# Performance work log

Measured on AMD Instinct MI355X. Metric: run time of the kernel, lower is better.

## Reference

```python
import jax, jax.numpy as jnp
import numpy as np

T, MEM, B, DM, N, D = 1024, 1024, 4, 1024, 16, 64
C = MEM + T
SCALE = 1.0 / D ** 0.5
LN_EPS = 1e-5


def _rel_shift(x):
    # x: [T, C, B, N] -> Transformer-XL relative shift
    t, c = x.shape[0], x.shape[1]
    zero_pad = jnp.zeros((t, 1) + x.shape[2:], x.dtype)
    x_padded = jnp.concatenate([zero_pad, x], axis=1)  # [T, C+1, B, N]
    x_padded = x_padded.reshape((c + 1, t) + x.shape[2:])
    return x_padded[1:].reshape(x.shape)


def setup_inputs() -> dict:
    key = jax.random.key(0)
    ks = jax.random.split(key, 8)
    h = jax.random.normal(ks[0], (T, B, DM), jnp.float32)
    m = jax.random.normal(ks[1], (MEM, B, DM), jnp.float32)
    r = jax.random.normal(ks[2], (C, DM), jnp.float32)
    # causal mask with memory: query i (global pos MEM+i) may attend to j <= MEM+i
    mask = (jnp.arange(C)[None, :] > (jnp.arange(T)[:, None] + MEM))[:, :, None]  # [T,C,1] bool, True=disallow
    W_qkv = jax.random.normal(ks[3], (DM, 3 * N * D), jnp.float32) * 0.02
    W_r = jax.random.normal(ks[4], (DM, N * D), jnp.float32) * 0.02
    W_o = jax.random.normal(ks[5], (N * D, DM), jnp.float32) * 0.02
    r_w_bias = jax.random.normal(ks[6], (N, D), jnp.float32)
    r_r_bias = jax.random.normal(ks[7], (N, D), jnp.float32)
    ln_gamma = jnp.ones((DM,), jnp.float32)
    ln_beta = jnp.zeros((DM,), jnp.float32)
    return {"h": h, "m": m, "r": r, "mask": mask, "W_qkv": W_qkv, "W_r": W_r,
            "W_o": W_o, "r_w_bias": r_w_bias, "r_r_bias": r_r_bias,
            "ln_gamma": ln_gamma, "ln_beta": ln_beta}


def reference(h, m, r, mask, W_qkv, W_r, W_o, r_w_bias, r_r_bias, ln_gamma, ln_beta):
    t, b = h.shape[0], h.shape[1]
    c = r.shape[0]
    cat = jnp.concatenate([m, h], axis=0)          # [C, B, DM]
    w_heads = cat @ W_qkv                           # [C, B, 3*N*D]
    w_q, w_k, w_v = jnp.split(w_heads, 3, axis=-1)
    w_q = w_q[-t:].reshape(t, b, N, D)              # [T,B,N,D]
    w_k = w_k.reshape(c, b, N, D)                   # [C,B,N,D]
    w_v = w_v.reshape(c, b, N, D)                   # [C,B,N,D]
    r_k = (r @ W_r).reshape(c, N, D)                # [C,N,D]
    AC = jnp.einsum('ibnd,jbnd->ijbn', w_q + r_w_bias, w_k)
    BD = jnp.einsum('ibnd,jnd->ijbn', w_q + r_r_bias, r_k)
    BD = _rel_shift(BD)
    score = (AC + BD) * SCALE                       # [T,C,B,N]
    score = jnp.where(mask[:, :, :, None], jnp.float32(-65000.0), score.astype(jnp.float32)).astype(score.dtype)
    prob = jax.nn.softmax(score, axis=1)
    vec = jnp.einsum('ijbn,jbnd->ibnd', prob, w_v).reshape(t, b, N * D)
    attn_out = vec @ W_o                            # [T,B,DM]
    x = h + attn_out
    mu = jnp.mean(x, axis=-1, keepdims=True)
    var = jnp.mean((x - mu) ** 2, axis=-1, keepdims=True)
    return (x - mu) * jax.lax.rsqrt(var + LN_EPS) * ln_gamma + ln_beta
```

## Files before the change

### kernel.cpp

```cpp
#include <hip/hip_runtime.h>
#include <stdint.h>

#define T_LEN 1024
#define MEM_LEN 1024
#define C_LEN 2048
#define B_SZ 4
#define DM_ 1024
#define NH 16
#define HD 64

typedef __attribute__((ext_vector_type(8))) short short8;
typedef __attribute__((ext_vector_type(4))) float f32x4;
typedef __attribute__((ext_vector_type(4))) unsigned short ushort4v;
typedef __attribute__((ext_vector_type(8))) unsigned short ushort8v;
typedef __attribute__((ext_vector_type(4))) float float4v;

__device__ __forceinline__ unsigned short f2bf(float f) {
  union { float f; unsigned int u; } v; v.f = f;
  unsigned int r = v.u + 0x7fffu + ((v.u >> 16) & 1u);
  return (unsigned short)(r >> 16);
}
__device__ __forceinline__ float bf2f(unsigned short b) {
  union { unsigned int u; float f; } v; v.u = ((unsigned int)b) << 16;
  return v.f;
}
__device__ __forceinline__ unsigned int cvtpk(float lo, float hi) {
  unsigned int r;
  asm("v_cvt_pk_bf16_f32 %0, %1, %2" : "=v"(r) : "v"(lo), "v"(hi));
  return r;
}
__device__ __forceinline__ f32x4 mfma16(short8 a, short8 b, f32x4 c) {
  return __builtin_amdgcn_mfma_f32_16x16x32_bf16(a, b, c, 0, 0, 0);
}

__global__ void k_convert_all(const float* __restrict__ m, const float* __restrict__ h,
                              const float* __restrict__ r,
                              unsigned short* __restrict__ catB,
                              unsigned short* __restrict__ rB) {
  int idx = blockIdx.x * 256 + threadIdx.x;
  const int MQ = (MEM_LEN * B_SZ * DM_) / 4;
  const int CQ = 2 * MQ;
  float4v v;
  unsigned short* dst;
  int di;
  if (idx < MQ)      { v = ((const float4v*)m)[idx];       dst = catB; di = idx; }
  else if (idx < CQ) { v = ((const float4v*)h)[idx - MQ];  dst = catB; di = idx; }
  else               { v = ((const float4v*)r)[idx - CQ];  dst = rB;   di = idx - CQ; }
  ushort4v o;
  o.x = f2bf(v.x); o.y = f2bf(v.y); o.z = f2bf(v.z); o.w = f2bf(v.w);
  ((ushort4v*)dst)[di] = o;
}

__global__ void k_transpose_w(const float* __restrict__ Wqkv, const float* __restrict__ Wr,
                              const float* __restrict__ Wo,
                              unsigned short* __restrict__ WqkvT, unsigned short* __restrict__ WrT,
                              unsigned short* __restrict__ WoT) {
  __shared__ float tile[32][33];
  const int z = blockIdx.z;
  const int Ccols = (z == 0) ? 3072 : 1024;
  if (blockIdx.x * 32 >= Ccols) return;
  const float* in = (z == 0) ? Wqkv : (z == 1) ? Wr : Wo;
  unsigned short* out = (z == 0) ? WqkvT : (z == 1) ? WrT : WoT;
  int c0 = blockIdx.x * 32, r0 = blockIdx.y * 32;
  int tx = threadIdx.x & 31, ty = threadIdx.x >> 5;
#pragma unroll
  for (int p = 0; p < 4; ++p)
    tile[ty + 8 * p][tx] = in[(size_t)(r0 + ty + 8 * p) * Ccols + c0 + tx];
  __syncthreads();
#pragma unroll
  for (int p = 0; p < 4; ++p)
    out[(size_t)(c0 + ty + 8 * p) * 1024 + r0 + tx] = f2bf(tile[tx][ty + 8 * p]);
}

template <int MODE>
__global__ __launch_bounds__(256) void k_gemm(const unsigned short* __restrict__ A,
                                              const unsigned short* __restrict__ BT,
                                              void* __restrict__ out1, void* __restrict__ out2,
                                              int M, int N, int K, int ldc) {
  __shared__ unsigned short As[128 * 64];
  __shared__ unsigned short Bs[128 * 64];
  const int tid = threadIdx.x;
  const int w = tid >> 6, l = tid & 63;
  const int wm = w >> 1, wn = w & 1;
  const int lg = l >> 4, lr = l & 15;
  const int gx = gridDim.x;
  const int pid = blockIdx.y * gx + blockIdx.x;
  const int xcd = pid & 7;
  const int idx = pid >> 3;
  const int cb = idx % gx;
  const int rb = (idx / gx) * 8 + xcd;
  const int m0 = rb * 128, n0 = cb * 128;
  f32x4 acc[4][4] = {};
  const int lrow8 = l >> 3;
  const int scol = (l & 7) * 8;
  const unsigned short* Abase = A + (size_t)m0 * K;
  const unsigned short* Bbase = BT + (size_t)n0 * K;
  for (int kt = 0; kt < K; kt += 64) {
    __syncthreads();
#pragma unroll
    for (int q = 0; q < 4; ++q) {
      int chunk = w * 4 + q;
      int row = chunk * 8 + lrow8;
      __builtin_amdgcn_global_load_lds(
          (const __attribute__((address_space(1))) void*)(Abase + (size_t)row * K + kt + scol),
          (__attribute__((address_space(3))) void*)(As + chunk * 512), 16, 0, 0);
      __builtin_amdgcn_global_load_lds(
          (const __attribute__((address_space(1))) void*)(Bbase + (size_t)row * K + kt + scol),
          (__attribute__((address_space(3))) void*)(Bs + chunk * 512), 16, 0, 0);
    }
    __syncthreads();
#pragma unroll
    for (int ks = 0; ks < 2; ++ks) {
      short8 a[4], bb[4];
#pragma unroll
      for (int mi = 0; mi < 4; ++mi)
        a[mi] = *(const short8*)&As[(wm * 64 + mi * 16 + lr) * 64 + ks * 32 + lg * 8];
#pragma unroll
      for (int ni = 0; ni < 4; ++ni)
        bb[ni] = *(const short8*)&Bs[(wn * 64 + ni * 16 + lr) * 64 + ks * 32 + lg * 8];
#pragma unroll
      for (int mi = 0; mi < 4; ++mi)
#pragma unroll
        for (int ni = 0; ni < 4; ++ni)
          acc[mi][ni] = mfma16(a[mi], bb[ni], acc[mi][ni]);
    }
  }
#pragma unroll
  for (int mi = 0; mi < 4; ++mi)
#pragma unroll
    for (int ni = 0; ni < 4; ++ni)
#pragma unroll
      for (int r = 0; r < 4; ++r) {
        int row = m0 + wm * 64 + mi * 16 + lg * 4 + r;
        int cc = n0 + wn * 64 + ni * 16 + lr;
        float val = acc[mi][ni][r];
        if (MODE == 1) {
          ((float*)out1)[(size_t)row * ldc + cc] = val;
        } else if (MODE == 2) {
          int nn = (cc & 1023) >> 6, d = cc & 63;
          int c = row >> 2, b = row & 3;
          size_t addr = ((size_t)((b * 16 + nn) * 2048 + c)) * 64 + d;
          unsigned short* dst = (cc < 1024) ? (unsigned short*)out1 : (unsigned short*)out2;
          dst[addr] = f2bf(val);
        } else if (MODE == 3) {
          int nn = cc >> 6, d = cc & 63;
          int t = row >> 2, b = row & 3;
          ((unsigned short*)out1)[((size_t)((b * 16 + nn) * 1024 + t)) * 64 + d] = f2bf(val);
        } else {
          int nn = cc >> 6, d = cc & 63;
          ((unsigned short*)out1)[((size_t)(nn * 2048 + row)) * 64 + d] = f2bf(val);
        }
      }
}

__global__ void k_vt(const unsigned short* __restrict__ Vp, unsigned short* __restrict__ VT) {
  __shared__ unsigned short tile[64][72];
  int c0 = blockIdx.x * 64;
  int n = blockIdx.y, b = blockIdx.z;
  int t = threadIdx.x;
  const unsigned short* src = Vp + ((size_t)((b * 16 + n) * 2048 + c0)) * 64;
#pragma unroll
  for (int p = 0; p < 16; ++p) {
    int idx = p * 256 + t;
    int r = idx >> 6, d = idx & 63;
    tile[d][r] = src[(size_t)r * 64 + d];
  }
  __syncthreads();
#pragma unroll
  for (int p = 0; p < 16; ++p) {
    int idx = p * 256 + t;
    int d = idx >> 6, c = idx & 63;
    VT[(size_t)((b * 16 + n) * 64 + d) * 2048 + c0 + c] = tile[d][c];
  }
}

__device__ __forceinline__ void stage_tile(const unsigned short* __restrict__ Kbase,
                                           const unsigned short* __restrict__ Vbase,
                                           unsigned short* ksBuf, unsigned short* vsBuf,
                                           int j0, int tid) {
#pragma unroll
  for (int q = 0; q < 2; ++q) {
    int chunk = q * 256 + tid;
    int row = chunk >> 3;
    int slot = chunk & 7;
    int ss = slot ^ (row & 7);
    __builtin_amdgcn_global_load_lds(
        (const __attribute__((address_space(1))) void*)(Kbase + (size_t)(j0 + row) * 64 + ss * 8),
        (__attribute__((address_space(3))) void*)(ksBuf + chunk * 8), 16, 0, 0);
    __builtin_amdgcn_global_load_lds(
        (const __attribute__((address_space(1))) void*)(Vbase + (size_t)row * 2048 + j0 + ss * 8),
        (__attribute__((address_space(3))) void*)(vsBuf + chunk * 8), 16, 0, 0);
  }
}

__global__ __launch_bounds__(256) void k_attn(const unsigned short* __restrict__ Qp,
                                              const unsigned short* __restrict__ Kp,
                                              const unsigned short* __restrict__ VT,
                                              const unsigned short* __restrict__ Rkp,
                                              const float* __restrict__ rwb,
                                              const float* __restrict__ rrb,
                                              unsigned short* __restrict__ po,
                                              float* __restrict__ psumG) {
  __shared__ __align__(16) unsigned short Ks[2][64 * 64];
  __shared__ __align__(16) unsigned short Vs[2][64 * 64];
  __shared__ unsigned short P[4][16][72];
  const int tid = threadIdx.x;
  const int w = tid >> 6, l = tid & 63;
  const int lg = l >> 4, lr = l & 15;
  const int L = blockIdx.x;
  const int bnlo = L & 7;
  const int rest = L >> 3;
  const int bnhi = rest / 48;
  const int inner = rest - bnhi * 48;
  const int xt = inner / 3;
  const int s  = inner - xt * 3;
  const int bn = bnhi * 8 + bnlo;
  const int i0 = xt * 64;
  const int n = bn & 15, b = bn >> 4;
  const int wrow = i0 + w * 16;

  const int ntile = xt + 17;
  const int t0 = (s * ntile) / 3;
  const int t1 = ((s + 1) * ntile) / 3;

  const unsigned short* Kbase = Kp + (size_t)bn * 2048 * 64;
  const unsigned short* Vbase = VT + (size_t)bn * 64 * 2048;
  const unsigned short* Rkbase = Rkp + (size_t)n * 2048 * 64;

  short8 aq0u, aq1u, aq0v, aq1v;
  {
    const unsigned short* qp = Qp + (size_t)(bn * 1024 + wrow + lr) * 64 + lg * 8;
    short8 q0 = *(const short8*)qp;
    short8 q1 = *(const short8*)(qp + 32);
    const float* up = rwb + n * 64 + lg * 8;
    const float* vp = rrb + n * 64 + lg * 8;
#pragma unroll
    for (int e = 0; e < 8; ++e) {
      float q0f = bf2f((unsigned short)q0[e]);
      float q1f = bf2f((unsigned short)q1[e]);
      aq0u[e] = (short)f2bf(q0f + up[e]);
      aq1u[e] = (short)f2bf(q1f + up[e + 32]);
      aq0v[e] = (short)f2bf(q0f + vp[e]);
      aq1v[e] = (short)f2bf(q1f + vp[e + 32]);
    }
  }
  float psum[4];
  f32x4 o[4];
#pragma unroll
  for (int r = 0; r < 4; ++r) psum[r] = 0.f;
#pragma unroll
  for (int df = 0; df < 4; ++df) o[df] = (f32x4){0.f, 0.f, 0.f, 0.f};

  stage_tile(Kbase, Vbase, Ks[0], Vs[0], t0 * 64, tid);
  stage_tile(Kbase, Vbase, Ks[1], Vs[1], (t0 + 1) * 64, tid);

  const float EXPC = 0.18033688011112042f;

  for (int jt = t0; jt < t1; ++jt) {
    const int j0 = jt * 64;
    const int cur = (jt - t0) & 1;
    if (jt + 1 < t1) { asm volatile("s_waitcnt vmcnt(4)" ::: "memory"); }
    else             { asm volatile("s_waitcnt vmcnt(0)" ::: "memory"); }
    __builtin_amdgcn_s_barrier();

    f32x4 sac[4];
#pragma unroll
    for (int jf = 0; jf < 4; ++jf) sac[jf] = (f32x4){0.f, 0.f, 0.f, 0.f};
    __builtin_amdgcn_s_setprio(1);
#pragma unroll
    for (int jf = 0; jf < 4; ++jf) {
      int row = jf * 16 + lr;
      int rx = row & 7;
      short8 k0 = *(const short8*)&Ks[cur][row * 64 + ((lg ^ rx) * 8)];
      short8 k1 = *(const short8*)&Ks[cur][row * 64 + (((4 + lg) ^ rx) * 8)];
      sac[jf] = mfma16(aq0u, k0, sac[jf]);
      sac[jf] = mfma16(aq1u, k1, sac[jf]);
    }
    __builtin_amdgcn_s_setprio(0);
    const int kbw = j0 + 1008 - i0 - w * 16;
    f32x4 gb[5];
#pragma unroll
    for (int jg = 0; jg < 5; ++jg) {
      int rowK = kbw + jg * 16 + lr;
      short8 b0 = {}, b1 = {};
      if (rowK < C_LEN) {
        const unsigned short* rp = Rkbase + (size_t)rowK * 64 + lg * 8;
        b0 = *(const short8*)rp;
        b1 = *(const short8*)(rp + 32);
      }
      f32x4 g = (f32x4){0.f, 0.f, 0.f, 0.f};
      g = mfma16(aq0v, b0, g);
      g = mfma16(aq1v, b1, g);
      gb[jg] = g;
    }
    const bool needMask = (j0 + 63 > i0 + w * 16 + MEM_LEN);
    float p[4][4];
#pragma unroll
    for (int r = 0; r < 4; ++r) {
      const int R = lg * 4 + r;
      const int delta = lr + 15 - R;
      const int src = (l & 48) | (delta & 15);
      float v0 = __shfl(gb[0][r], src);
      float v1 = __shfl(gb[1][r], src);
      float v2 = __shfl(gb[2][r], src);
      float v3 = __shfl(gb[3][r], src);
      float v4 = __shfl(gb[4][r], src);
      const bool hi = delta >= 16;
      float bd0 = hi ? v1 : v0;
      float bd1 = hi ? v2 : v1;
      float bd2 = hi ? v3 : v2;
      float bd3 = hi ? v4 : v3;
      float e0 = exp2f((sac[0][r] + bd0) * EXPC);
      float e1 = exp2f((sac[1][r] + bd1) * EXPC);
      float e2 = exp2f((sac[2][r] + bd2) * EXPC);
      float e3 = exp2f((sac[3][r] + bd3) * EXPC);
      if (needMask) {
        const int jlim = i0 + w * 16 + R + MEM_LEN;
        int j = j0 + lr;
        e0 = (j > jlim) ? 0.f : e0;  j += 16;
        e1 = (j > jlim) ? 0.f : e1;  j += 16;
        e2 = (j > jlim) ? 0.f : e2;  j += 16;
        e3 = (j > jlim) ? 0.f : e3;
      }
      p[0][r] = e0; p[1][r] = e1; p[2][r] = e2; p[3][r] = e3;
    }
#pragma unroll
    for (int jf = 0; jf < 4; ++jf)
#pragma unroll
      for (int r = 0; r < 4; ++r) psum[r] += p[jf][r];
#pragma unroll
    for (int r = 0; r < 4; ++r) {
      unsigned int a01 = cvtpk(p[0][r], p[1][r]);
      unsigned int a23 = cvtpk(p[2][r], p[3][r]);
      const int R = lg * 4 + r;
      P[w][R][lr]      = (unsigned short)a01;
      P[w][R][16 + lr] = (unsigned short)(a01 >> 16);
      P[w][R][32 + lr] = (unsigned short)a23;
      P[w][R][48 + lr] = (unsigned short)(a23 >> 16);
    }
    __builtin_amdgcn_s_setprio(1);
#pragma unroll
    for (int ks = 0; ks < 2; ++ks) {
      short8 ap = *(const short8*)&P[w][lr][ks * 32 + lg * 8];
#pragma unroll
      for (int df = 0; df < 4; ++df) {
        int row = df * 16 + lr;
        int rx = row & 7;
        short8 vv = *(const short8*)&Vs[cur][row * 64 + (((ks * 4 + lg) ^ rx) * 8)];
        o[df] = mfma16(ap, vv, o[df]);
      }
    }
    __builtin_amdgcn_s_setprio(0);
    __builtin_amdgcn_s_barrier();
    if (jt + 2 < t1)
      stage_tile(Kbase, Vbase, Ks[cur], Vs[cur], (jt + 2) * 64, tid);
  }
  const int pbase = (bn * 16 + xt) * 3 + s;
  unsigned short* poB = po + (size_t)pbase * 4096;
#pragma unroll
  for (int r = 0; r < 4; ++r) {
    float v = psum[r];
    v += __shfl_xor(v, 1);
    v += __shfl_xor(v, 2);
    v += __shfl_xor(v, 4);
    v += __shfl_xor(v, 8);
    if (lr == 0) psumG[pbase * 64 + w * 16 + lg * 4 + r] = v;
  }
#pragma unroll
  for (int df = 0; df < 4; ++df)
#pragma unroll
    for (int r = 0; r < 4; ++r)
      poB[(w * 16 + lg * 4 + r) * 64 + df * 16 + lr] = f2bf(o[df][r]);
}

__global__ __launch_bounds__(256) void k_ared(const unsigned short* __restrict__ po,
                                              const float* __restrict__ psumG,
                                              unsigned short* __restrict__ vec) {
  const int idx = blockIdx.x;
  const int tid = threadIdx.x;
  const int bn = idx >> 4, xt = idx & 15;
  const int b = bn >> 4, n = bn & 15;
  __shared__ float rs[64];
  if (tid < 64) {
    const float* q = psumG + idx * 192;
    rs[tid] = q[tid] + q[tid + 64] + q[tid + 128];
  }
  __syncthreads();
  const ushort8v* p0 = (const ushort8v*)(po + (size_t)(idx * 3 + 0) * 4096);
  const ushort8v* p1 = (const ushort8v*)(po + (size_t)(idx * 3 + 1) * 4096);
  const ushort8v* p2 = (const ushort8v*)(po + (size_t)(idx * 3 + 2) * 4096);
#pragma unroll
  for (int k = 0; k < 2; ++k) {
    int e = tid + k * 256;
    int row = e >> 3, d8 = e & 7;
    ushort8v a = p0[e], bb = p1[e], c = p2[e];
    float inv = 1.f / rs[row];
    int t = xt * 64 + row;
    ushort8v ov;
#pragma unroll
    for (int q = 0; q < 8; ++q)
      ov[q] = f2bf((bf2f(a[q]) + bf2f(bb[q]) + bf2f(c[q])) * inv);
    *(ushort8v*)&vec[(size_t)(t * 4 + b) * 1024 + n * 64 + d8 * 8] = ov;
  }
}

__global__ __launch_bounds__(256) void k_ln(const float* __restrict__ xg, const float* __restrict__ h,
                                            const float* __restrict__ gamma, const float* __restrict__ beta,
                                            float* __restrict__ out) {
  const int row = blockIdx.x;
  const int t = threadIdx.x;
  __shared__ float red1[4], red2[4];
  float4v xv = ((const float4v*)(xg + (size_t)row * 1024))[t];
  float4v hv = ((const float4v*)(h + (size_t)row * 1024))[t];
  float x0 = xv.x + hv.x, x1 = xv.y + hv.y, x2 = xv.z + hv.z, x3 = xv.w + hv.w;
  float s = x0 + x1 + x2 + x3;
#pragma unroll
  for (int off = 1; off < 64; off <<= 1) s += __shfl_xor(s, off);
  if ((t & 63) == 0) red1[t >> 6] = s;
  __syncthreads();
  float mean = (red1[0] + red1[1] + red1[2] + red1[3]) * (1.f / 1024.f);
  float d0 = x0 - mean, d1 = x1 - mean, d2 = x2 - mean, d3 = x3 - mean;
  float q = d0 * d0 + d1 * d1 + d2 * d2 + d3 * d3;
#pragma unroll
  for (int off = 1; off < 64; off <<= 1) q += __shfl_xor(q, off);
  if ((t & 63) == 0) red2[t >> 6] = q;
  __syncthreads();
  float var = (red2[0] + red2[1] + red2[2] + red2[3]) * (1.f / 1024.f);
  float rs = rsqrtf(var + 1e-5f);
  float4v gv = ((const float4v*)gamma)[t];
  float4v bv = ((const float4v*)beta)[t];
  float4v ov;
  ov.x = d0 * rs * gv.x + bv.x;
  ov.y = d1 * rs * gv.y + bv.y;
  ov.z = d2 * rs * gv.z + bv.z;
  ov.w = d3 * rs * gv.w + bv.w;
  ((float4v*)(out + (size_t)row * 1024))[t] = ov;
}

extern "C" void kernel_launch(void* const* d_in, const int* in_sizes, int n_in,
                              void* d_out, int out_size, void* d_ws, size_t ws_size,
                              hipStream_t stream) {
  (void)in_sizes; (void)n_in; (void)out_size; (void)ws_size;
  const float* h    = (const float*)d_in[0];
  const float* m    = (const float*)d_in[1];
  const float* r    = (const float*)d_in[2];
  const float* Wqkv = (const float*)d_in[4];
  const float* Wr   = (const float*)d_in[5];
  const float* Wo   = (const float*)d_in[6];
  const float* rwb  = (const float*)d_in[7];
  const float* rrb  = (const float*)d_in[8];
  const float* gam  = (const float*)d_in[9];
  const float* bet  = (const float*)d_in[10];
  float* out = (float*)d_out;

  char* ws = (char*)d_ws;
  unsigned short* catB   = (unsigned short*)(ws + 0);
  unsigned short* WqkvT  = (unsigned short*)(ws + 16777216);
  unsigned short* WrT    = (unsigned short*)(ws + 23068672);
  unsigned short* WoT    = (unsigned short*)(ws + 25165824);
  unsigned short* Vp     = (unsigned short*)(ws + 27262976);
  unsigned short* po     = (unsigned short*)(ws + 44040192);
  unsigned short* VT     = (unsigned short*)(ws + 81788928);
  unsigned short* vec    = (unsigned short*)(ws + 99221504);
  float* xbuf            = (float*)(ws + 107610112);
  unsigned short* rB     = (unsigned short*)(ws + 124387328);
  unsigned short* Kp     = (unsigned short*)(ws + 128581632);
  unsigned short* Qp     = (unsigned short*)(ws + 145358848);
  unsigned short* Rkp    = (unsigned short*)(ws + 153747456);
  float* psumG = (float*)(ws + 124387328);

  hipLaunchKernelGGL(k_convert_all, dim3(10240), dim3(256), 0, stream, m, h, r, catB, rB);
  hipLaunchKernelGGL(k_transpose_w, dim3(96, 32, 3), dim3(256), 0, stream,
                     Wqkv, Wr, Wo, WqkvT, WrT, WoT);
  hipLaunchKernelGGL(k_gemm<2>, dim3(16, 64), dim3(256), 0, stream,
                     catB, WqkvT + (size_t)1024 * 1024, (void*)Kp, (void*)Vp, 8192, 2048, 1024, 0);
  hipLaunchKernelGGL(k_gemm<3>, dim3(8, 32), dim3(256), 0, stream,
                     catB + (size_t)4096 * 1024, WqkvT, (void*)Qp, nullptr, 4096, 1024, 1024, 0);
  hipLaunchKernelGGL(k_gemm<4>, dim3(8, 16), dim3(256), 0, stream,
                     rB, WrT, (void*)Rkp, nullptr, 2048, 1024, 1024, 0);
  hipLaunchKernelGGL(k_vt, dim3(32, 16, 4), dim3(256), 0, stream, Vp, VT);
  hipLaunchKernelGGL(k_attn, dim3(3072), dim3(256), 0, stream, Qp, Kp, VT, Rkp, rwb, rrb, po, psumG);
  hipLaunchKernelGGL(k_ared, dim3(1024), dim3(256), 0, stream, po, psumG, vec);
  hipLaunchKernelGGL(k_gemm<1>, dim3(8, 32), dim3(256), 0, stream,
                     vec, WoT, (void*)xbuf, nullptr, 4096, 1024, 1024, 1024);
  hipLaunchKernelGGL(k_ln, dim3(4096), dim3(256), 0, stream, xbuf, h, gam, bet, out);
}
```

Baseline: 322.9 us.

## Merge QKV/R projection GEMMs into one launch and single-buffer V in attention

The three projection GEMMs (K/V, Q, R) are merged into one grouped launch of 1408 blocks, with the block index choosing the mode. This removes two launch tails and lets the small GEMMs fill the GPU alongside the large one. In the attention kernel, V becomes single-buffered and is staged one tile ahead, separately from K, which stays double-buffered. An extra waitcnt and barrier before the PV MFMA step cut LDS use, possibly raising occupancy, at the cost of exposing V load latency and an extra barrier per tile. The s_setprio hints are also removed.

```diff
diff --git a/kernel.cpp b/kernel.cpp
--- a/kernel.cpp
+++ b/kernel.cpp
@@ -72,11 +72,96 @@
     out[(size_t)(c0 + ty + 8 * p) * 1024 + r0 + tx] = f2bf(tile[tx][ty + 8 * p]);
 }
 
-template <int MODE>
-__global__ __launch_bounds__(256) void k_gemm(const unsigned short* __restrict__ A,
-                                              const unsigned short* __restrict__ BT,
-                                              void* __restrict__ out1, void* __restrict__ out2,
-                                              int M, int N, int K, int ldc) {
+__global__ __launch_bounds__(256) void k_gemm_qkv(const unsigned short* __restrict__ catB,
+                                                  const unsigned short* __restrict__ rB,
+                                                  const unsigned short* __restrict__ WqkvT,
+                                                  const unsigned short* __restrict__ WrT,
+                                                  unsigned short* __restrict__ Kp,
+                                                  unsigned short* __restrict__ Vp,
+                                                  unsigned short* __restrict__ Qp,
+                                                  unsigned short* __restrict__ Rkp) {
+  __shared__ unsigned short As[128 * 64];
+  __shared__ unsigned short Bs[128 * 64];
+  const int tid = threadIdx.x;
+  const int w = tid >> 6, l = tid & 63;
+  const int wm = w >> 1, wn = w & 1;
+  const int lg = l >> 4, lr = l & 15;
+  const int bid = blockIdx.x;
+  int mode, lpid, gx;
+  const unsigned short *A, *BT;
+  if (bid < 1024)      { mode = 2; lpid = bid;        gx = 16; A = catB;                        BT = WqkvT + (size_t)1024 * 1024; }
+  else if (bid < 1280) { mode = 3; lpid = bid - 1024; gx = 8;  A = catB + (size_t)4096 * 1024;  BT = WqkvT; }
+  else                 { mode = 4; lpid = bid - 1280; gx = 8;  A = rB;                          BT = WrT; }
+  const int K = 1024;
+  const int xcd = lpid & 7;
+  const int idx = lpid >> 3;
+  const int cb = idx % gx;
+  const int rb = (idx / gx) * 8 + xcd;
+  const int m0 = rb * 128, n0 = cb * 128;
+  f32x4 acc[4][4] = {};
+  const int lrow8 = l >> 3;
+  const int scol = (l & 7) * 8;
+  const unsigned short* Abase = A + (size_t)m0 * K;
+  const unsigned short* Bbase = BT + (size_t)n0 * K;
+  for (int kt = 0; kt < K; kt += 64) {
+    __syncthreads();
+#pragma unroll
+    for (int q = 0; q < 4; ++q) {
+      int chunk = w * 4 + q;
+      int row = chunk * 8 + lrow8;
+      __builtin_amdgcn_global_load_lds(
+          (const __attribute__((address_space(1))) void*)(Abase + (size_t)row * K + kt + scol),
+          (__attribute__((address_space(3))) void*)(As + chunk * 512), 16, 0, 0);
+      __builtin_amdgcn_global_load_lds(
+          (const __attribute__((address_space(1))) void*)(Bbase + (size_t)row * K + kt + scol),
+          (__attribute__((address_space(3))) void*)(Bs + chunk * 512), 16, 0, 0);
+    }
+    __syncthreads();
+#pragma unroll
+    for (int ks = 0; ks < 2; ++ks) {
+      short8 a[4], bb[4];
+#pragma unroll
+      for (int mi = 0; mi < 4; ++mi)
+        a[mi] = *(const short8*)&As[(wm * 64 + mi * 16 + lr) * 64 + ks * 32 + lg * 8];
+#pragma unroll
+      for (int ni = 0; ni < 4; ++ni)
+        bb[ni] = *(const short8*)&Bs[(wn * 64 + ni * 16 + lr) * 64 + ks * 32 + lg * 8];
+#pragma unroll
+      for (int mi = 0; mi < 4; ++mi)
+#pragma unroll
+        for (int ni = 0; ni < 4; ++ni)
+          acc[mi][ni] = mfma16(a[mi], bb[ni], acc[mi][ni]);
+    }
+  }
+#pragma unroll
+  for (int mi = 0; mi < 4; ++mi)
+#pragma unroll
+    for (int ni = 0; ni < 4; ++ni)
+#pragma unroll
+      for (int r = 0; r < 4; ++r) {
+        int row = m0 + wm * 64 + mi * 16 + lg * 4 + r;
+        int cc = n0 + wn * 64 + ni * 16 + lr;
+        float val = acc[mi][ni][r];
+        if (mode == 2) {
+          int nn = (cc & 1023) >> 6, d = cc & 63;
+          int c = row >> 2, b = row & 3;
+          size_t addr = ((size_t)((b * 16 + nn) * 2048 + c)) * 64 + d;
+          unsigned short* dst = (cc < 1024) ? Kp : Vp;
+          dst[addr] = f2bf(val);
+        } else if (mode == 3) {
+          int nn = cc >> 6, d = cc & 63;
+          int t = row >> 2, b = row & 3;
+          Qp[((size_t)((b * 16 + nn) * 1024 + t)) * 64 + d] = f2bf(val);
+        } else {
+          int nn = cc >> 6, d = cc & 63;
+          Rkp[((size_t)(nn * 2048 + row)) * 64 + d] = f2bf(val);
+        }
+      }
+}
+
+__global__ __launch_bounds__(256) void k_gemm_o(const unsigned short* __restrict__ A,
+                                                const unsigned short* __restrict__ BT,
+                                                float* __restrict__ Cout, int M, int N, int K) {
   __shared__ unsigned short As[128 * 64];
   __shared__ unsigned short Bs[128 * 64];
   const int tid = threadIdx.x;
@@ -133,23 +218,7 @@
       for (int r = 0; r < 4; ++r) {
         int row = m0 + wm * 64 + mi * 16 + lg * 4 + r;
         int cc = n0 + wn * 64 + ni * 16 + lr;
-        float val = acc[mi][ni][r];
-        if (MODE == 1) {
-          ((float*)out1)[(size_t)row * ldc + cc] = val;
-        } else if (MODE == 2) {
-          int nn = (cc & 1023) >> 6, d = cc & 63;
-          int c = row >> 2, b = row & 3;
-          size_t addr = ((size_t)((b * 16 + nn) * 2048 + c)) * 64 + d;
-          unsigned short* dst = (cc < 1024) ? (unsigned short*)out1 : (unsigned short*)out2;
-          dst[addr] = f2bf(val);
-        } else if (MODE == 3) {
-          int nn = cc >> 6, d = cc & 63;
-          int t = row >> 2, b = row & 3;
-          ((unsigned short*)out1)[((size_t)((b * 16 + nn) * 1024 + t)) * 64 + d] = f2bf(val);
-        } else {
-          int nn = cc >> 6, d = cc & 63;
-          ((unsigned short*)out1)[((size_t)(nn * 2048 + row)) * 64 + d] = f2bf(val);
-        }
+        Cout[(size_t)row * N + cc] = acc[mi][ni][r];
       }
 }
 
@@ -174,10 +243,8 @@
   }
 }
 
-__device__ __forceinline__ void stage_tile(const unsigned short* __restrict__ Kbase,
-                                           const unsigned short* __restrict__ Vbase,
-                                           unsigned short* ksBuf, unsigned short* vsBuf,
-                                           int j0, int tid) {
+__device__ __forceinline__ void stage_k(const unsigned short* __restrict__ Kbase,
+                                        unsigned short* ksBuf, int j0, int tid) {
 #pragma unroll
   for (int q = 0; q < 2; ++q) {
     int chunk = q * 256 + tid;
@@ -187,6 +254,16 @@
     __builtin_amdgcn_global_load_lds(
         (const __attribute__((address_space(1))) void*)(Kbase + (size_t)(j0 + row) * 64 + ss * 8),
         (__attribute__((address_space(3))) void*)(ksBuf + chunk * 8), 16, 0, 0);
+  }
+}
+__device__ __forceinline__ void stage_v(const unsigned short* __restrict__ Vbase,
+                                        unsigned short* vsBuf, int j0, int tid) {
+#pragma unroll
+  for (int q = 0; q < 2; ++q) {
+    int chunk = q * 256 + tid;
+    int row = chunk >> 3;
+    int slot = chunk & 7;
+    int ss = slot ^ (row & 7);
     __builtin_amdgcn_global_load_lds(
         (const __attribute__((address_space(1))) void*)(Vbase + (size_t)row * 2048 + j0 + ss * 8),
         (__attribute__((address_space(3))) void*)(vsBuf + chunk * 8), 16, 0, 0);
@@ -202,7 +279,7 @@
                                               unsigned short* __restrict__ po,
                                               float* __restrict__ psumG) {
   __shared__ __align__(16) unsigned short Ks[2][64 * 64];
-  __shared__ __align__(16) unsigned short Vs[2][64 * 64];
+  __shared__ __align__(16) unsigned short Vs[64 * 64];
   __shared__ unsigned short P[4][16][72];
   const int tid = threadIdx.x;
   const int w = tid >> 6, l = tid & 63;
@@ -251,22 +328,23 @@
 #pragma unroll
   for (int df = 0; df < 4; ++df) o[df] = (f32x4){0.f, 0.f, 0.f, 0.f};
 
-  stage_tile(Kbase, Vbase, Ks[0], Vs[0], t0 * 64, tid);
-  stage_tile(Kbase, Vbase, Ks[1], Vs[1], (t0 + 1) * 64, tid);
+  stage_k(Kbase, Ks[0], t0 * 64, tid);
+  stage_v(Vbase, Vs, t0 * 64, tid);
+  stage_k(Kbase, Ks[1], (t0 + 1) * 64, tid);
 
   const float EXPC = 0.18033688011112042f;
 
   for (int jt = t0; jt < t1; ++jt) {
     const int j0 = jt * 64;
     const int cur = (jt - t0) & 1;
-    if (jt + 1 < t1) { asm volatile("s_waitcnt vmcnt(4)" ::: "memory"); }
-    else             { asm volatile("s_waitcnt vmcnt(0)" ::: "memory"); }
+    const bool more = (jt + 1 < t1);
+    if (more) { asm volatile("s_waitcnt vmcnt(4)" ::: "memory"); }
+    else      { asm volatile("s_waitcnt vmcnt(2)" ::: "memory"); }
     __builtin_amdgcn_s_barrier();
 
     f32x4 sac[4];
 #pragma unroll
     for (int jf = 0; jf < 4; ++jf) sac[jf] = (f32x4){0.f, 0.f, 0.f, 0.f};
-    __builtin_amdgcn_s_setprio(1);
 #pragma unroll
     for (int jf = 0; jf < 4; ++jf) {
       int row = jf * 16 + lr;
@@ -276,7 +354,6 @@
       sac[jf] = mfma16(aq0u, k0, sac[jf]);
       sac[jf] = mfma16(aq1u, k1, sac[jf]);
     }
-    __builtin_amdgcn_s_setprio(0);
     const int kbw = j0 + 1008 - i0 - w * 16;
     f32x4 gb[5];
 #pragma unroll
@@ -338,7 +415,9 @@
       P[w][R][32 + lr] = (unsigned short)a23;
       P[w][R][48 + lr] = (unsigned short)(a23 >> 16);
     }
-    __builtin_amdgcn_s_setprio(1);
+    if (more) { asm volatile("s_waitcnt vmcnt(2)" ::: "memory"); }
+    else      { asm volatile("s_waitcnt vmcnt(0)" ::: "memory"); }
+    __builtin_amdgcn_s_barrier();
 #pragma unroll
     for (int ks = 0; ks < 2; ++ks) {
       short8 ap = *(const short8*)&P[w][lr][ks * 32 + lg * 8];
@@ -346,14 +425,13 @@
       for (int df = 0; df < 4; ++df) {
         int row = df * 16 + lr;
         int rx = row & 7;
-        short8 vv = *(const short8*)&Vs[cur][row * 64 + (((ks * 4 + lg) ^ rx) * 8)];
+        short8 vv = *(const short8*)&Vs[row * 64 + (((ks * 4 + lg) ^ rx) * 8)];
         o[df] = mfma16(ap, vv, o[df]);
       }
     }
-    __builtin_amdgcn_s_setprio(0);
     __builtin_amdgcn_s_barrier();
-    if (jt + 2 < t1)
-      stage_tile(Kbase, Vbase, Ks[cur], Vs[cur], (jt + 2) * 64, tid);
+    if (jt + 1 < t1) stage_v(Vbase, Vs, (jt + 1) * 64, tid);
+    if (jt + 2 < t1) stage_k(Kbase, Ks[cur], (jt + 2) * 64, tid);
   }
   const int pbase = (bn * 16 + xt) * 3 + s;
   unsigned short* poB = po + (size_t)pbase * 4096;
@@ -472,16 +550,11 @@
   hipLaunchKernelGGL(k_convert_all, dim3(10240), dim3(256), 0, stream, m, h, r, catB, rB);
   hipLaunchKernelGGL(k_transpose_w, dim3(96, 32, 3), dim3(256), 0, stream,
                      Wqkv, Wr, Wo, WqkvT, WrT, WoT);
-  hipLaunchKernelGGL(k_gemm<2>, dim3(16, 64), dim3(256), 0, stream,
-                     catB, WqkvT + (size_t)1024 * 1024, (void*)Kp, (void*)Vp, 8192, 2048, 1024, 0);
-  hipLaunchKernelGGL(k_gemm<3>, dim3(8, 32), dim3(256), 0, stream,
-                     catB + (size_t)4096 * 1024, WqkvT, (void*)Qp, nullptr, 4096, 1024, 1024, 0);
-  hipLaunchKernelGGL(k_gemm<4>, dim3(8, 16), dim3(256), 0, stream,
-                     rB, WrT, (void*)Rkp, nullptr, 2048, 1024, 1024, 0);
+  hipLaunchKernelGGL(k_gemm_qkv, dim3(1408), dim3(256), 0, stream,
+                     catB, rB, WqkvT, WrT, Kp, Vp, Qp, Rkp);
   hipLaunchKernelGGL(k_vt, dim3(32, 16, 4), dim3(256), 0, stream, Vp, VT);
   hipLaunchKernelGGL(k_attn, dim3(3072), dim3(256), 0, stream, Qp, Kp, VT, Rkp, rwb, rrb, po, psumG);
   hipLaunchKernelGGL(k_ared, dim3(1024), dim3(256), 0, stream, po, psumG, vec);
-  hipLaunchKernelGGL(k_gemm<1>, dim3(8, 32), dim3(256), 0, stream,
-                     vec, WoT, (void*)xbuf, nullptr, 4096, 1024, 1024, 1024);
+  hipLaunchKernelGGL(k_gemm_o, dim3(8, 32), dim3(256), 0, stream, vec, WoT, xbuf, 4096, 1024, 1024);
   hipLaunchKernelGGL(k_ln, dim3(4096), dim3(256), 0, stream, xbuf, h, gam, bet, out);
 }
```

New measurement: 312.3 us. 3.3% less time.
